# Kernel optimization log

Measured on AMD Instinct MI355X. Metric: run time of the kernel, lower is better.

The kernel has to match this reference:

```python
import jax, jax.numpy as jnp
import numpy as np

E, H, FF, L, S, B = 64, 4, 32, 9, 7, 8192
HD = E // H


def setup_inputs() -> dict:
    key = jax.random.key(0)
    ks = iter(jax.random.split(key, 32))
    def rn(shape, scale=0.05):
        return jax.random.normal(next(ks), shape, dtype=jnp.float32) * scale
    inp = {
        "feature1": jax.random.normal(next(ks), (B, S, E), dtype=jnp.float32),
        "feature2": jax.random.normal(next(ks), (B, S, E), dtype=jnp.float32),
        # branch dim 2: index 0 = rotation, 1 = translation; then layer dim L
        "sa1_win": rn((2, L, 3 * E, E)), "sa1_bin": rn((2, L, 3 * E)),
        "sa1_wout": rn((2, L, E, E)), "sa1_bout": rn((2, L, E)),
        "sa2_win": rn((2, L, 3 * E, E)), "sa2_bin": rn((2, L, 3 * E)),
        "sa2_wout": rn((2, L, E, E)), "sa2_bout": rn((2, L, E)),
        "ca_win": rn((2, L, 3 * E, E)), "ca_bin": rn((2, L, 3 * E)),
        "ca_wout": rn((2, L, E, E)), "ca_bout": rn((2, L, E)),
        "ff_w1": rn((2, L, FF, E)), "ff_b1": rn((2, L, FF)),
        "ff_w2": rn((2, L, E, FF)), "ff_b2": rn((2, L, E)),
        "query_embed": jax.random.normal(next(ks), (2, S, E), dtype=jnp.float32),
        "fc_rot_w": rn((4, E)), "fc_rot_b": rn((4,)),
        "fc_trans_w": rn((3, E)), "fc_trans_b": rn((3,)),
    }
    return inp


def mha(q_in, kv_in, win, b_in, wout, bout):
    # torch nn.MultiheadAttention with batch_first=True
    wq, wk, wv = win[:E], win[E:2 * E], win[2 * E:]
    bq, bk, bv = b_in[:E], b_in[E:2 * E], b_in[2 * E:]
    b, sq, _ = q_in.shape
    sk = kv_in.shape[1]
    q = (q_in @ wq.T + bq).reshape(b, sq, H, HD)
    k = (kv_in @ wk.T + bk).reshape(b, sk, H, HD)
    v = (kv_in @ wv.T + bv).reshape(b, sk, H, HD)
    scores = jnp.einsum("bqhd,bkhd->bhqk", q, k) / jnp.sqrt(jnp.float32(HD))
    attn = jax.nn.softmax(scores, axis=-1)
    ctx = jnp.einsum("bhqk,bkhd->bqhd", attn, v).reshape(b, sq, E)
    return ctx @ wout.T + bout


def _branch(f1, f2, query, bi, sa1_win, sa1_bin, sa1_wout, sa1_bout,
            sa2_win, sa2_bin, sa2_wout, sa2_bout,
            ca_win, ca_bin, ca_wout, ca_bout, ff_w1, ff_b1, ff_w2, ff_b2):
    q = query
    for i in range(L):
        f1 = f1 + mha(f1, f1, sa1_win[bi, i], sa1_bin[bi, i], sa1_wout[bi, i], sa1_bout[bi, i])
        f2 = f2 + mha(f2, f2, sa2_win[bi, i], sa2_bin[bi, i], sa2_wout[bi, i], sa2_bout[bi, i])
        kv = jnp.concatenate([f1, f2], axis=1)  # (B, 2S, E)
        q = q + mha(q, kv, ca_win[bi, i], ca_bin[bi, i], ca_wout[bi, i], ca_bout[bi, i])
        h = jax.nn.relu(q @ ff_w1[bi, i].T + ff_b1[bi, i])
        q = q + h @ ff_w2[bi, i].T + ff_b2[bi, i]
    return q


def reference(feature1, feature2, sa1_win, sa1_bin, sa1_wout, sa1_bout,
              sa2_win, sa2_bin, sa2_wout, sa2_bout,
              ca_win, ca_bin, ca_wout, ca_bout,
              ff_w1, ff_b1, ff_w2, ff_b2, query_embed,
              fc_rot_w, fc_rot_b, fc_trans_w, fc_trans_b):
    b = feature1.shape[0]
    args = (sa1_win, sa1_bin, sa1_wout, sa1_bout, sa2_win, sa2_bin, sa2_wout,
            sa2_bout, ca_win, ca_bin, ca_wout, ca_bout, ff_w1, ff_b1, ff_w2, ff_b2)
    q_rot = jnp.broadcast_to(query_embed[0][None], (b, S, E))
    q_trn = jnp.broadcast_to(query_embed[1][None], (b, S, E))
    # rotation and translation branches are mathematically independent
    rot = _branch(feature1, feature2, q_rot, 0, *args)
    trn = _branch(feature1, feature2, q_trn, 1, *args)
    pose_rot = (rot @ fc_rot_w.T + fc_rot_b).mean(axis=1)    # (B, 4)
    pose_trn = (trn @ fc_trans_w.T + fc_trans_b).mean(axis=1)  # (B, 3)
    return jnp.concatenate([pose_rot, pose_trn], axis=1)  # (B, 7)
```

## Files before the change

kernel.cpp:

```cpp
#include <hip/hip_runtime.h>
#include <hip/hip_bf16.h>

namespace {

using bf16x8 = __attribute__((ext_vector_type(8))) short;
using f32x4  = __attribute__((ext_vector_type(4))) float;

constexpr int NL = 9, S = 7, BB = 8192;
constexpr int G = 8;
constexpr int M = G * S;
constexpr int NT = 512;

constexpr int OFF_F1 = 0;
constexpr int OFF_F2 = 14336;
constexpr int OFF_Q  = 28672;
constexpr int OFF_QB = 43008;
constexpr int OFF_KB = 50176;
constexpr int OFF_VT = 64512;
constexpr int SMEM_TOTAL = 80896;

__device__ __forceinline__ unsigned short f2bf(float f) {
  union { __hip_bfloat16 h; unsigned short s; } u;
  u.h = __float2bfloat16(f);
  return u.s;
}
__device__ __forceinline__ uint32_t pk2(float a, float b) {
  return (uint32_t)f2bf(a) | ((uint32_t)f2bf(b) << 16);
}
__device__ __forceinline__ int swzS(int r, int c) {
  return r * 256 + ((((c >> 3) ^ (r & 7)) << 5) | ((c & 7) << 2));
}
__device__ __forceinline__ int swzB(int r, int c) {
  return r * 128 + ((((c >> 3) ^ (r & 7)) << 4) | ((c & 7) << 1));
}
__device__ __forceinline__ int swzV(int d, int kv) {
  return d * 256 + ((((kv >> 3) ^ (d & 7)) << 4) | ((kv & 7) << 1));
}
__device__ __forceinline__ int div7(int t) { return (t * 9363) >> 16; }

__device__ __forceinline__ bf16x8 ldStateFrag(const char* base, int r, int k0) {
  const float4* p = (const float4*)(base + r * 256 + (((k0 >> 3) ^ (r & 7)) << 5));
  float4 x = p[0], y = p[1];
  union { bf16x8 v; uint32_t u[4]; } o;
  o.u[0] = pk2(x.x, x.y); o.u[1] = pk2(x.z, x.w);
  o.u[2] = pk2(y.x, y.y); o.u[3] = pk2(y.z, y.w);
  return o.v;
}
__device__ __forceinline__ bf16x8 ldBfFrag(const char* base, int r, int k0) {
  return *(const bf16x8*)(base + r * 128 + (((k0 >> 3) ^ (r & 7)) << 4));
}

struct StvNone { __device__ void operator()(int, int, f32x4) const {} };

template <int MTOT, int NTOT, int KF, int WMG, int WNG, int VNT, bool WS,
          class BLD, class STN, class STV>
__device__ __forceinline__ void gemm_sw(const short* __restrict__ wbf,
                                        const float* __restrict__ wf,
                                        const float* __restrict__ bias,
                                        int ldK, int wid, int lane,
                                        BLD bld, STN stn, STV stv)
{
  const int wm = wid / WNG, wn = wid % WNG;
  const int q = lane & 15, gI = lane >> 4;
  constexpr int MPW = (MTOT + WMG - 1) / WMG;
  constexpr int NPW = NTOT / WNG;
  bf16x8 bfr[MPW][KF];
#pragma unroll
  for (int i = 0; i < MPW; ++i) {
    const int mt = wm * MPW + i;
    if (mt < MTOT) {
#pragma unroll
      for (int kf = 0; kf < KF; ++kf)
        bfr[i][kf] = bld(mt * 16 + q, kf * 32 + gI * 8);
    }
  }
#pragma unroll
  for (int j = 0; j < NPW; ++j) {
    const int nt = wn * NPW + j;
    bf16x8 afr[KF];
#pragma unroll
    for (int kf = 0; kf < KF; ++kf) {
      const int k0 = kf * 32 + gI * 8;
      if constexpr (WS) {
        afr[kf] = *(const bf16x8*)(wbf + (size_t)(nt * 16 + q) * ldK + k0);
      } else {
        const float* wp = wf + (size_t)(nt * 16 + q) * ldK + k0;
        float4 x = *(const float4*)wp, y = *(const float4*)(wp + 4);
        union { bf16x8 v; uint32_t u[4]; } o;
        o.u[0] = pk2(x.x, x.y); o.u[1] = pk2(x.z, x.w);
        o.u[2] = pk2(y.x, y.y); o.u[3] = pk2(y.z, y.w);
        afr[kf] = o.v;
      }
    }
    if (nt < VNT) {
      const float4 b4 = *(const float4*)(bias + nt * 16 + gI * 4);
#pragma unroll
      for (int i = 0; i < MPW; ++i) {
        const int mt = wm * MPW + i;
        if (mt < MTOT) {
          f32x4 acc = { b4.x, b4.y, b4.z, b4.w };
#pragma unroll
          for (int kf = 0; kf < KF; ++kf)
            acc = __builtin_amdgcn_mfma_f32_16x16x32_bf16(afr[kf], bfr[i][kf], acc, 0, 0, 0);
          stn(mt, nt, acc);
        }
      }
    } else {
      const float bv = bias[nt * 16 + q];
#pragma unroll
      for (int i = 0; i < MPW; ++i) {
        const int mt = wm * MPW + i;
        if (mt < MTOT) {
          f32x4 acc = { bv, bv, bv, bv };
#pragma unroll
          for (int kf = 0; kf < KF; ++kf)
            acc = __builtin_amdgcn_mfma_f32_16x16x32_bf16(bfr[i][kf], afr[kf], acc, 0, 0, 0);
          stv(mt, nt, acc);
        }
      }
    }
  }
}

template <bool CA_>
__device__ __forceinline__ void attn(char* qb, const char* kb, const char* vt,
                                     int wid, int lane)
{
  const int q = lane & 15, gI = lane >> 4;
  const int g = wid;
  constexpr int KVL = CA_ ? 14 : 7;
#pragma unroll
  for (int h = 0; h < 4; ++h) {
    bf16x8 kfrag = {}, qfrag = {};
    if (gI < 2) {
      int qrow = g * 7 + q; qrow = qrow > 55 ? 55 : qrow;
      qfrag = ldBfFrag(qb, qrow, h * 16 + gI * 8);
      int kvr;
      if constexpr (CA_) {
        kvr = (q < 7) ? (g * 7 + q) : (49 + g * 7 + q);
        kvr = kvr > 111 ? 111 : kvr;
      } else {
        kvr = g * 7 + q; kvr = kvr > 55 ? 55 : kvr;
      }
      kfrag = ldBfFrag(kb, kvr, h * 16 + gI * 8);
    }
    f32x4 s = { 0.f, 0.f, 0.f, 0.f };
    s = __builtin_amdgcn_mfma_f32_16x16x32_bf16(kfrag, qfrag, s, 0, 0, 0);

    float e[4]; float sum = 0.f;
#pragma unroll
    for (int jj = 0; jj < 4; ++jj) {
      const int kvloc = gI * 4 + jj;
      const float tt = fminf(s[jj] * 0.36067376f, 60.f);
      e[jj] = (kvloc < KVL) ? exp2f(tt) : 0.f;
      sum += e[jj];
    }
    sum += __shfl_xor(sum, 16);
    sum += __shfl_xor(sum, 32);
    const float inv = __builtin_amdgcn_rcpf(sum);

    union { bf16x8 v; uint32_t u[4]; } pb;
    pb.u[0] = pk2(e[0] * inv, e[1] * inv);
    pb.u[1] = pk2(e[2] * inv, e[3] * inv);
    pb.u[2] = 0; pb.u[3] = 0;

    const int d = h * 16 + q;
    const int kv0 = (CA_ ? g * 16 : g * 8) + gI * 4;
    const uint2 vv = *(const uint2*)(vt + swzV(d, kv0));
    union { bf16x8 v; uint32_t u[4]; } va;
    va.u[0] = vv.x; va.u[1] = vv.y; va.u[2] = 0; va.u[3] = 0;

    f32x4 o = { 0.f, 0.f, 0.f, 0.f };
    o = __builtin_amdgcn_mfma_f32_16x16x32_bf16(va.v, pb.v, o, 0, 0, 0);

    if (q < 7) {
      const int tok = g * 7 + q, c0 = h * 16 + gI * 4;
      *(uint2*)(qb + swzB(tok, c0)) = make_uint2(pk2(o[0], o[1]), pk2(o[2], o[3]));
    }
  }
}

template <class BLD, bool WS>
__device__ __forceinline__ void out_proj(char* ST, const short* Wo, const float* Fo,
                                         const float* Bo, int wid, int lane, BLD bldc)
{
  const int q = lane & 15, gI = lane >> 4;
  auto stres = [&](int mt, int nt, f32x4 a) {
    const int tok = mt * 16 + q; if (tok >= M) return;
    const int c0 = nt * 16 + gI * 4;
    float4* p = (float4*)(ST + tok * 256 + (((c0 >> 3) ^ (tok & 7)) << 5) + (c0 & 7) * 4);
    float4 v = *p;
    v.x += a[0]; v.y += a[1]; v.z += a[2]; v.w += a[3];
    *p = v;
  };
  gemm_sw<4, 4, 2, 2, 4, 4, WS>(Wo, Fo, Bo, 64, wid, lane, bldc, stres, StvNone{});
}

template <bool WS>
__device__ __forceinline__ void sa_block(char* ST, char* qb, char* kb, char* vt,
    const short* Wi, const float* Fi, const float* Bi,
    const short* Wo, const float* Fo, const float* Bo,
    int wid, int lane)
{
  const int q = lane & 15, gI = lane >> 4;
  auto bld = [&](int r, int k0) { return ldStateFrag(ST, r > 55 ? 55 : r, k0); };
  auto stn = [&](int mt, int nt, f32x4 a) {
    const int tok = mt * 16 + q; if (tok >= M) return;
    if (nt < 4) {
      *(uint2*)(qb + swzB(tok, nt * 16 + gI * 4)) =
          make_uint2(pk2(a[0], a[1]), pk2(a[2], a[3]));
    } else {
      *(uint2*)(kb + swzB(tok, (nt - 4) * 16 + gI * 4)) =
          make_uint2(pk2(a[0], a[1]), pk2(a[2], a[3]));
    }
  };
  auto stv = [&](int mt, int nt, f32x4 a) {
    const int d = (nt - 8) * 16 + q;
#pragma unroll
    for (int jj = 0; jj < 4; ++jj) {
      const int tok = mt * 16 + gI * 4 + jj;
      if (tok < M) {
        const int g = div7(tok);
        *(short*)(vt + swzV(d, g * 8 + (tok - g * 7))) = (short)f2bf(a[jj]);
      }
    }
  };
  gemm_sw<4, 12, 2, 2, 4, 8, WS>(Wi, Fi, Bi, 64, wid, lane, bld, stn, stv);
  __syncthreads();
  attn<false>(qb, kb, vt, wid, lane);
  __syncthreads();
  auto bldc = [&](int r, int k0) { return ldBfFrag(qb, r > 55 ? 55 : r, k0); };
  out_proj<decltype(bldc), WS>(ST, Wo, Fo, Bo, wid, lane, bldc);
  __syncthreads();
}

template <bool WS, int SRC>
__device__ __forceinline__ void ca_kv(const char* SS, char* kb, char* vt,
    const short* Wi, const float* Fi, const float* Bi, int wid, int lane)
{
  const int q = lane & 15, gI = lane >> 4;
  auto bld = [&](int r, int k0) { return ldStateFrag(SS, r > 55 ? 55 : r, k0); };
  auto stk = [&](int mt, int nt, f32x4 a) {
    const int tok = mt * 16 + q; if (tok >= M) return;
    *(uint2*)(kb + swzB(tok + SRC * 56, nt * 16 + gI * 4)) =
        make_uint2(pk2(a[0], a[1]), pk2(a[2], a[3]));
  };
  auto stv = [&](int mt, int nt, f32x4 a) {
    const int d = (nt - 4) * 16 + q;
#pragma unroll
    for (int jj = 0; jj < 4; ++jj) {
      const int tok = mt * 16 + gI * 4 + jj;
      if (tok < M) {
        const int g = div7(tok);
        *(short*)(vt + swzV(d, g * 16 + (tok - g * 7) + SRC * 7)) = (short)f2bf(a[jj]);
      }
    }
  };
  gemm_sw<4, 8, 2, 2, 4, 4, WS>(Wi + 4096, Fi + 4096, Bi + 64, 64, wid, lane,
                                bld, stk, stv);
}

template <bool WS>
__global__ __launch_bounds__(NT, 4) void pose_kernel(
    const float* __restrict__ feature1, const float* __restrict__ feature2,
    const float* __restrict__ sa1_win, const float* __restrict__ sa1_bin,
    const float* __restrict__ sa1_wout, const float* __restrict__ sa1_bout,
    const float* __restrict__ sa2_win, const float* __restrict__ sa2_bin,
    const float* __restrict__ sa2_wout, const float* __restrict__ sa2_bout,
    const float* __restrict__ ca_win, const float* __restrict__ ca_bin,
    const float* __restrict__ ca_wout, const float* __restrict__ ca_bout,
    const float* __restrict__ ff_w1, const float* __restrict__ ff_b1,
    const float* __restrict__ ff_w2, const float* __restrict__ ff_b2,
    const float* __restrict__ query_embed,
    const float* __restrict__ fc_rot_w, const float* __restrict__ fc_rot_b,
    const float* __restrict__ fc_trans_w, const float* __restrict__ fc_trans_b,
    const short* __restrict__ wbf, float* __restrict__ out)
{
  extern __shared__ char smem[];
  char* sF1 = smem + OFF_F1;
  char* sF2 = smem + OFF_F2;
  char* sQ  = smem + OFF_Q;
  char* qb  = smem + OFF_QB;
  char* kb  = smem + OFF_KB;
  char* vt  = smem + OFF_VT;

  const int t = threadIdx.x;
  const int wid = t >> 6, lane = t & 63;
  const int q = lane & 15, gI = lane >> 4;
  const int bi = blockIdx.y;
  const int b0 = blockIdx.x * G;

  {
    const uint4 z = { 0, 0, 0, 0 };
    for (int i = t; i < 1024; i += NT) ((uint4*)vt)[i] = z;
  }
  {
    const float* f1p = feature1 + (size_t)b0 * (S * 64);
    const float* f2p = feature2 + (size_t)b0 * (S * 64);
    const float* qe  = query_embed + (size_t)bi * (S * 64);
    for (int idx = t; idx < M * 64; idx += NT) {
      const int r = idx >> 6, c = idx & 63;
      const int s = r - div7(r) * 7;
      *(float*)(sF1 + swzS(r, c)) = f1p[idx];
      *(float*)(sF2 + swzS(r, c)) = f2p[idx];
      *(float*)(sQ + swzS(r, c))  = qe[s * 64 + c];
    }
  }
  __syncthreads();

  for (int li = 0; li < NL; ++li) {
    const int wo = bi * NL + li;

    sa_block<WS>(sF1, qb, kb, vt,
                 wbf + wo * 12288,          sa1_win + wo * 12288,  sa1_bin + wo * 192,
                 wbf + 663552 + wo * 4096,  sa1_wout + wo * 4096,  sa1_bout + wo * 64,
                 wid, lane);
    sa_block<WS>(sF2, qb, kb, vt,
                 wbf + 221184 + wo * 12288, sa2_win + wo * 12288,  sa2_bin + wo * 192,
                 wbf + 737280 + wo * 4096,  sa2_wout + wo * 4096,  sa2_bout + wo * 64,
                 wid, lane);

    {
      const short* Wi = wbf + 442368 + wo * 12288;
      const float* Fi = ca_win + wo * 12288;
      const float* Bi = ca_bin + wo * 192;
      auto bldq = [&](int r, int k0) { return ldStateFrag(sQ, r > 55 ? 55 : r, k0); };
      auto stq = [&](int mt, int nt, f32x4 a) {
        const int tok = mt * 16 + q; if (tok >= M) return;
        *(uint2*)(qb + swzB(tok, nt * 16 + gI * 4)) =
            make_uint2(pk2(a[0], a[1]), pk2(a[2], a[3]));
      };
      gemm_sw<4, 4, 2, 2, 4, 4, WS>(Wi, Fi, Bi, 64, wid, lane, bldq, stq, StvNone{});
      ca_kv<WS, 0>(sF1, kb, vt, Wi, Fi, Bi, wid, lane);
      ca_kv<WS, 1>(sF2, kb, vt, Wi, Fi, Bi, wid, lane);
      __syncthreads();
      attn<true>(qb, kb, vt, wid, lane);
      __syncthreads();
      auto bldc = [&](int r, int k0) { return ldBfFrag(qb, r > 55 ? 55 : r, k0); };
      out_proj<decltype(bldc), WS>(sQ, wbf + 811008 + wo * 4096, ca_wout + wo * 4096,
                                   ca_bout + wo * 64, wid, lane, bldc);
      __syncthreads();
    }

    {
      auto bldq = [&](int r, int k0) { return ldStateFrag(sQ, r > 55 ? 55 : r, k0); };
      auto sth = [&](int mt, int nt, f32x4 a) {
        const int tok = mt * 16 + q; if (tok >= M) return;
        *(uint2*)(qb + swzB(tok, nt * 16 + gI * 4)) =
            make_uint2(pk2(fmaxf(a[0], 0.f), fmaxf(a[1], 0.f)),
                       pk2(fmaxf(a[2], 0.f), fmaxf(a[3], 0.f)));
      };
      gemm_sw<4, 2, 2, 4, 2, 2, WS>(wbf + 884736 + wo * 2048, ff_w1 + wo * 2048,
                                    ff_b1 + wo * 32, 64, wid, lane, bldq, sth, StvNone{});
      __syncthreads();
      auto bldh = [&](int r, int k0) { return ldBfFrag(qb, r > 55 ? 55 : r, k0); };
      auto stres = [&](int mt, int nt, f32x4 a) {
        const int tok = mt * 16 + q; if (tok >= M) return;
        const int c0 = nt * 16 + gI * 4;
        float4* p = (float4*)(sQ + tok * 256 + (((c0 >> 3) ^ (tok & 7)) << 5) + (c0 & 7) * 4);
        float4 v = *p;
        v.x += a[0]; v.y += a[1]; v.z += a[2]; v.w += a[3];
        *p = v;
      };
      gemm_sw<4, 4, 1, 2, 4, 4, WS>(wbf + 921600 + wo * 2048, ff_w2 + wo * 2048,
                                    ff_b2 + wo * 64, 32, wid, lane, bldh, stres, StvNone{});
      __syncthreads();
    }
  }

  float* cs = (float*)qb;
  {
    const int g = t >> 6, c = t & 63;
    float a = 0.f;
#pragma unroll
    for (int s = 0; s < 7; ++s) a += *(const float*)(sQ + swzS(g * 7 + s, c));
    cs[t] = a;
  }
  __syncthreads();
  const int ncols = bi ? 3 : 4;
  if (t < G * ncols) {
    const int g = t / ncols, cc = t - g * ncols;
    const float* wv = bi ? (fc_trans_w + cc * 64) : (fc_rot_w + cc * 64);
    float acc = 0.f;
#pragma unroll
    for (int k = 0; k < 64; ++k) acc += cs[g * 64 + k] * wv[k];
    const float bb = bi ? fc_trans_b[cc] : fc_rot_b[cc];
    out[(size_t)(b0 + g) * 7 + (bi ? 4 : 0) + cc] = acc * (1.f / 7.f) + bb;
  }
}

__global__ void prep_kernel(const float* __restrict__ a0, const float* __restrict__ a1,
                            const float* __restrict__ a2, const float* __restrict__ a3,
                            const float* __restrict__ a4, const float* __restrict__ a5,
                            const float* __restrict__ a6, const float* __restrict__ a7,
                            short* __restrict__ dst)
{
  for (int i = blockIdx.x * blockDim.x + threadIdx.x; i < 958464;
       i += gridDim.x * blockDim.x) {
    const float* s; int j;
    if      (i < 221184) { s = a0; j = i; }
    else if (i < 442368) { s = a1; j = i - 221184; }
    else if (i < 663552) { s = a2; j = i - 442368; }
    else if (i < 737280) { s = a3; j = i - 663552; }
    else if (i < 811008) { s = a4; j = i - 737280; }
    else if (i < 884736) { s = a5; j = i - 811008; }
    else if (i < 921600) { s = a6; j = i - 884736; }
    else                 { s = a7; j = i - 921600; }
    dst[i] = (short)f2bf(s[j]);
  }
}

}

extern "C" void kernel_launch(void* const* d_in, const int* in_sizes, int n_in,
                              void* d_out, int out_size, void* d_ws, size_t ws_size,
                              hipStream_t stream)
{
  const float* feature1    = (const float*)d_in[0];
  const float* feature2    = (const float*)d_in[1];
  const float* sa1_win     = (const float*)d_in[2];
  const float* sa1_bin     = (const float*)d_in[3];
  const float* sa1_wout    = (const float*)d_in[4];
  const float* sa1_bout    = (const float*)d_in[5];
  const float* sa2_win     = (const float*)d_in[6];
  const float* sa2_bin     = (const float*)d_in[7];
  const float* sa2_wout    = (const float*)d_in[8];
  const float* sa2_bout    = (const float*)d_in[9];
  const float* ca_win      = (const float*)d_in[10];
  const float* ca_bin      = (const float*)d_in[11];
  const float* ca_wout     = (const float*)d_in[12];
  const float* ca_bout     = (const float*)d_in[13];
  const float* ff_w1       = (const float*)d_in[14];
  const float* ff_b1       = (const float*)d_in[15];
  const float* ff_w2       = (const float*)d_in[16];
  const float* ff_b2       = (const float*)d_in[17];
  const float* query_embed = (const float*)d_in[18];
  const float* fc_rot_w    = (const float*)d_in[19];
  const float* fc_rot_b    = (const float*)d_in[20];
  const float* fc_trans_w  = (const float*)d_in[21];
  const float* fc_trans_b  = (const float*)d_in[22];

  const bool ws_ok = (d_ws != nullptr) && (ws_size >= (size_t)958464 * 2);
  dim3 grid(BB / G, 2);

  if (ws_ok) {
    prep_kernel<<<dim3(936), 512, 0, stream>>>(sa1_win, sa2_win, ca_win,
                                               sa1_wout, sa2_wout, ca_wout,
                                               ff_w1, ff_w2, (short*)d_ws);
    hipFuncSetAttribute(reinterpret_cast<const void*>(&pose_kernel<true>),
                        hipFuncAttributeMaxDynamicSharedMemorySize, SMEM_TOTAL);
    pose_kernel<true><<<grid, NT, SMEM_TOTAL, stream>>>(
        feature1, feature2,
        sa1_win, sa1_bin, sa1_wout, sa1_bout,
        sa2_win, sa2_bin, sa2_wout, sa2_bout,
        ca_win, ca_bin, ca_wout, ca_bout,
        ff_w1, ff_b1, ff_w2, ff_b2,
        query_embed, fc_rot_w, fc_rot_b, fc_trans_w, fc_trans_b,
        (const short*)d_ws, (float*)d_out);
  } else {
    hipFuncSetAttribute(reinterpret_cast<const void*>(&pose_kernel<false>),
                        hipFuncAttributeMaxDynamicSharedMemorySize, SMEM_TOTAL);
    pose_kernel<false><<<grid, NT, SMEM_TOTAL, stream>>>(
        feature1, feature2,
        sa1_win, sa1_bin, sa1_wout, sa1_bout,
        sa2_win, sa2_bin, sa2_wout, sa2_bout,
        ca_win, ca_bin, ca_wout, ca_bout,
        ff_w1, ff_b1, ff_w2, ff_b2,
        query_embed, fc_rot_w, fc_rot_b, fc_trans_w, fc_trans_b,
        (const short*)d_ws, (float*)d_out);
  }
}
```

Baseline: 1.350 ms.

## Give each wavefront its own batch sample and drop block-wide barriers

Restructures the kernel so each of the 8 waves in a block processes one batch element independently, with its own LDS region. Block-level __syncthreads are replaced by compiler memory fences, and the V layout and attention masking are simplified for a single sample. Each wave now runs all N-tiles of every GEMM on one 16-row M tile with only 7 valid rows, which wastes more MFMA work per sample and multiplies weight fragment loads per sample. In exchange it removes cross-wave synchronization. The final pose head is also reduced with wave shuffles.

Measured after the change: 2.342 ms. +73.5%, slower.

```diff
diff --git a/kernel.cpp b/kernel.cpp
--- a/kernel.cpp
+++ b/kernel.cpp
@@ -1,23 +1,25 @@
 #include <hip/hip_runtime.h>
 #include <hip/hip_bf16.h>
 
+#define WAVE_FENCE() asm volatile("" ::: "memory")
+
 namespace {
 
 using bf16x8 = __attribute__((ext_vector_type(8))) short;
 using f32x4  = __attribute__((ext_vector_type(4))) float;
 
-constexpr int NL = 9, S = 7, BB = 8192;
-constexpr int G = 8;
-constexpr int M = G * S;
-constexpr int NT = 512;
-
-constexpr int OFF_F1 = 0;
-constexpr int OFF_F2 = 14336;
-constexpr int OFF_Q  = 28672;
-constexpr int OFF_QB = 43008;
-constexpr int OFF_KB = 50176;
-constexpr int OFF_VT = 64512;
-constexpr int SMEM_TOTAL = 80896;
+constexpr int NL = 9, BB = 8192;
+constexpr int WPB = 8;
+constexpr int NT = 64 * WPB;
+
+constexpr int WV_F1 = 0;
+constexpr int WV_F2 = 1792;
+constexpr int WV_SQ = 3584;
+constexpr int WV_QB = 5376;
+constexpr int WV_KB = 6272;
+constexpr int WV_VT = 8192;
+constexpr int WVSZ  = 10240;
+constexpr int SMEM_TOTAL = WVSZ * WPB;
 
 __device__ __forceinline__ unsigned short f2bf(float f) {
   union { __hip_bfloat16 h; unsigned short s; } u;
@@ -33,10 +35,6 @@
 __device__ __forceinline__ int swzB(int r, int c) {
   return r * 128 + ((((c >> 3) ^ (r & 7)) << 4) | ((c & 7) << 1));
 }
-__device__ __forceinline__ int swzV(int d, int kv) {
-  return d * 256 + ((((kv >> 3) ^ (d & 7)) << 4) | ((kv & 7) << 1));
-}
-__device__ __forceinline__ int div7(int t) { return (t * 9363) >> 16; }
 
 __device__ __forceinline__ bf16x8 ldStateFrag(const char* base, int r, int k0) {
   const float4* p = (const float4*)(base + r * 256 + (((k0 >> 3) ^ (r & 7)) << 5));
@@ -47,126 +45,112 @@
   return o.v;
 }
 __device__ __forceinline__ bf16x8 ldBfFrag(const char* base, int r, int k0) {
-  return *(const bf16x8*)(base + r * 128 + (((k0 >> 3) ^ (r & 7)) << 4));
-}
-
-struct StvNone { __device__ void operator()(int, int, f32x4) const {} };
-
-template <int MTOT, int NTOT, int KF, int WMG, int WNG, int VNT, bool WS,
-          class BLD, class STN, class STV>
-__device__ __forceinline__ void gemm_sw(const short* __restrict__ wbf,
-                                        const float* __restrict__ wf,
-                                        const float* __restrict__ bias,
-                                        int ldK, int wid, int lane,
-                                        BLD bld, STN stn, STV stv)
-{
-  const int wm = wid / WNG, wn = wid % WNG;
-  const int q = lane & 15, gI = lane >> 4;
-  constexpr int MPW = (MTOT + WMG - 1) / WMG;
-  constexpr int NPW = NTOT / WNG;
-  bf16x8 bfr[MPW][KF];
+  const uint2* p = (const uint2*)(base + r * 128 + (((k0 >> 3) ^ (r & 7)) << 4));
+  const uint2 a = p[0], b = p[1];
+  union { bf16x8 v; uint32_t u[4]; } o;
+  o.u[0] = a.x; o.u[1] = a.y; o.u[2] = b.x; o.u[3] = b.y;
+  return o.v;
+}
+
+template <int NTOT, int KF, int VNT, bool WS, class BLD, class STN, class STV>
+__device__ __forceinline__ void gemmw(const short* __restrict__ wbf,
+                                      const float* __restrict__ wf,
+                                      const float* __restrict__ biasN,
+                                      const float* __restrict__ biasV,
+                                      int q, int gI, BLD bld, STN stn, STV stv)
+{
+  constexpr int LDK = (KF == 2) ? 64 : 32;
+  const bf16x8 b0 = bld(q, gI * 8);
+  bf16x8 b1 = b0;
+  if constexpr (KF == 2) b1 = bld(q, 32 + gI * 8);
 #pragma unroll
-  for (int i = 0; i < MPW; ++i) {
-    const int mt = wm * MPW + i;
-    if (mt < MTOT) {
-#pragma unroll
-      for (int kf = 0; kf < KF; ++kf)
-        bfr[i][kf] = bld(mt * 16 + q, kf * 32 + gI * 8);
-    }
-  }
-#pragma unroll
-  for (int j = 0; j < NPW; ++j) {
-    const int nt = wn * NPW + j;
-    bf16x8 afr[KF];
-#pragma unroll
-    for (int kf = 0; kf < KF; ++kf) {
-      const int k0 = kf * 32 + gI * 8;
-      if constexpr (WS) {
-        afr[kf] = *(const bf16x8*)(wbf + (size_t)(nt * 16 + q) * ldK + k0);
-      } else {
-        const float* wp = wf + (size_t)(nt * 16 + q) * ldK + k0;
+  for (int nt = 0; nt < NTOT; ++nt) {
+    const int row = nt * 16 + q;
+    bf16x8 a0, a1;
+    if constexpr (WS) {
+      a0 = *(const bf16x8*)(wbf + row * LDK + gI * 8);
+      if constexpr (KF == 2)
+        a1 = *(const bf16x8*)(wbf + row * LDK + 32 + gI * 8);
+    } else {
+      {
+        const float* wp = wf + row * LDK + gI * 8;
         float4 x = *(const float4*)wp, y = *(const float4*)(wp + 4);
         union { bf16x8 v; uint32_t u[4]; } o;
         o.u[0] = pk2(x.x, x.y); o.u[1] = pk2(x.z, x.w);
         o.u[2] = pk2(y.x, y.y); o.u[3] = pk2(y.z, y.w);
-        afr[kf] = o.v;
+        a0 = o.v;
       }
+      a1 = a0;
+      if constexpr (KF == 2) {
+        const float* wp = wf + row * LDK + 32 + gI * 8;
+        float4 x = *(const float4*)wp, y = *(const float4*)(wp + 4);
+        union { bf16x8 v; uint32_t u[4]; } o;
+        o.u[0] = pk2(x.x, x.y); o.u[1] = pk2(x.z, x.w);
+        o.u[2] = pk2(y.x, y.y); o.u[3] = pk2(y.z, y.w);
+        a1 = o.v;
+      }
     }
     if (nt < VNT) {
-      const float4 b4 = *(const float4*)(bias + nt * 16 + gI * 4);
-#pragma unroll
-      for (int i = 0; i < MPW; ++i) {
-        const int mt = wm * MPW + i;
-        if (mt < MTOT) {
-          f32x4 acc = { b4.x, b4.y, b4.z, b4.w };
-#pragma unroll
-          for (int kf = 0; kf < KF; ++kf)
-            acc = __builtin_amdgcn_mfma_f32_16x16x32_bf16(afr[kf], bfr[i][kf], acc, 0, 0, 0);
-          stn(mt, nt, acc);
-        }
-      }
+      const float4 b4 = *(const float4*)(biasN + nt * 16 + gI * 4);
+      f32x4 acc = { b4.x, b4.y, b4.z, b4.w };
+      acc = __builtin_amdgcn_mfma_f32_16x16x32_bf16(a0, b0, acc, 0, 0, 0);
+      if constexpr (KF == 2)
+        acc = __builtin_amdgcn_mfma_f32_16x16x32_bf16(a1, b1, acc, 0, 0, 0);
+      stn(nt, acc);
     } else {
-      const float bv = bias[nt * 16 + q];
-#pragma unroll
-      for (int i = 0; i < MPW; ++i) {
-        const int mt = wm * MPW + i;
-        if (mt < MTOT) {
-          f32x4 acc = { bv, bv, bv, bv };
-#pragma unroll
-          for (int kf = 0; kf < KF; ++kf)
-            acc = __builtin_amdgcn_mfma_f32_16x16x32_bf16(bfr[i][kf], afr[kf], acc, 0, 0, 0);
-          stv(mt, nt, acc);
-        }
-      }
+      const float bv = biasV[(nt - VNT) * 16 + q];
+      f32x4 acc = { bv, bv, bv, bv };
+      acc = __builtin_amdgcn_mfma_f32_16x16x32_bf16(b0, a0, acc, 0, 0, 0);
+      if constexpr (KF == 2)
+        acc = __builtin_amdgcn_mfma_f32_16x16x32_bf16(b1, a1, acc, 0, 0, 0);
+      stv(nt - VNT, acc);
     }
   }
 }
 
 template <bool CA_>
-__device__ __forceinline__ void attn(char* qb, const char* kb, const char* vt,
-                                     int wid, int lane)
-{
-  const int q = lane & 15, gI = lane >> 4;
-  const int g = wid;
-  constexpr int KVL = CA_ ? 14 : 7;
+__device__ __forceinline__ void attnw(char* qb, const char* kb, const char* vt,
+                                      int q, int gI)
+{
+  constexpr int KCL = CA_ ? 14 : 6;
 #pragma unroll
   for (int h = 0; h < 4; ++h) {
     bf16x8 kfrag = {}, qfrag = {};
     if (gI < 2) {
-      int qrow = g * 7 + q; qrow = qrow > 55 ? 55 : qrow;
-      qfrag = ldBfFrag(qb, qrow, h * 16 + gI * 8);
-      int kvr;
-      if constexpr (CA_) {
-        kvr = (q < 7) ? (g * 7 + q) : (49 + g * 7 + q);
-        kvr = kvr > 111 ? 111 : kvr;
-      } else {
-        kvr = g * 7 + q; kvr = kvr > 55 ? 55 : kvr;
-      }
-      kfrag = ldBfFrag(kb, kvr, h * 16 + gI * 8);
+      qfrag = ldBfFrag(qb, q > 6 ? 6 : q, h * 16 + gI * 8);
+      kfrag = ldBfFrag(kb, q > KCL ? KCL : q, h * 16 + gI * 8);
     }
     f32x4 s = { 0.f, 0.f, 0.f, 0.f };
     s = __builtin_amdgcn_mfma_f32_16x16x32_bf16(kfrag, qfrag, s, 0, 0, 0);
 
-    float e[4]; float sum = 0.f;
-#pragma unroll
-    for (int jj = 0; jj < 4; ++jj) {
-      const int kvloc = gI * 4 + jj;
-      const float tt = fminf(s[jj] * 0.36067376f, 60.f);
-      e[jj] = (kvloc < KVL) ? exp2f(tt) : 0.f;
-      sum += e[jj];
+    float e0, e1, e2, e3, sum;
+    {
+      const int k0 = gI * 4;
+      const float t0 = fminf(s[0] * 0.36067376f, 60.f);
+      const float t1 = fminf(s[1] * 0.36067376f, 60.f);
+      const float t2 = fminf(s[2] * 0.36067376f, 60.f);
+      const float t3 = fminf(s[3] * 0.36067376f, 60.f);
+      const bool v0 = CA_ ? (((k0 + 0) & 7) < 7) : (k0 + 0 < 7);
+      const bool v1 = CA_ ? (((k0 + 1) & 7) < 7) : (k0 + 1 < 7);
+      const bool v2 = CA_ ? (((k0 + 2) & 7) < 7) : (k0 + 2 < 7);
+      const bool v3 = CA_ ? (((k0 + 3) & 7) < 7) : (k0 + 3 < 7);
+      e0 = v0 ? exp2f(t0) : 0.f;
+      e1 = v1 ? exp2f(t1) : 0.f;
+      e2 = v2 ? exp2f(t2) : 0.f;
+      e3 = v3 ? exp2f(t3) : 0.f;
+      sum = e0 + e1 + e2 + e3;
     }
     sum += __shfl_xor(sum, 16);
     sum += __shfl_xor(sum, 32);
     const float inv = __builtin_amdgcn_rcpf(sum);
 
     union { bf16x8 v; uint32_t u[4]; } pb;
-    pb.u[0] = pk2(e[0] * inv, e[1] * inv);
-    pb.u[1] = pk2(e[2] * inv, e[3] * inv);
+    pb.u[0] = pk2(e0 * inv, e1 * inv);
+    pb.u[1] = pk2(e2 * inv, e3 * inv);
     pb.u[2] = 0; pb.u[3] = 0;
 
     const int d = h * 16 + q;
-    const int kv0 = (CA_ ? g * 16 : g * 8) + gI * 4;
-    const uint2 vv = *(const uint2*)(vt + swzV(d, kv0));
+    const uint2 vv = *(const uint2*)(vt + d * 32 + gI * 8);
     union { bf16x8 v; uint32_t u[4]; } va;
     va.u[0] = vv.x; va.u[1] = vv.y; va.u[2] = 0; va.u[3] = 0;
 
@@ -174,90 +158,63 @@
     o = __builtin_amdgcn_mfma_f32_16x16x32_bf16(va.v, pb.v, o, 0, 0, 0);
 
     if (q < 7) {
-      const int tok = g * 7 + q, c0 = h * 16 + gI * 4;
-      *(uint2*)(qb + swzB(tok, c0)) = make_uint2(pk2(o[0], o[1]), pk2(o[2], o[3]));
-    }
-  }
-}
-
-template <class BLD, bool WS>
-__device__ __forceinline__ void out_proj(char* ST, const short* Wo, const float* Fo,
-                                         const float* Bo, int wid, int lane, BLD bldc)
-{
-  const int q = lane & 15, gI = lane >> 4;
-  auto stres = [&](int mt, int nt, f32x4 a) {
-    const int tok = mt * 16 + q; if (tok >= M) return;
+      *(uint2*)(qb + swzB(q, h * 16 + gI * 4)) =
+          make_uint2(pk2(o[0], o[1]), pk2(o[2], o[3]));
+    }
+  }
+}
+
+template <bool WS>
+__device__ __forceinline__ void sa_blockw(char* ST, char* qb, char* kb, char* vt,
+    const short* Wi, const float* Fi, const float* Bi,
+    const short* Wo, const float* Fo, const float* Bo, int q, int gI)
+{
+  auto bld = [&](int r, int k0) { return ldStateFrag(ST, r > 6 ? 6 : r, k0); };
+  auto stn = [&](int nt, f32x4 a) {
+    if (q >= 7) return;
+    const uint2 v = make_uint2(pk2(a[0], a[1]), pk2(a[2], a[3]));
+    if (nt < 4) *(uint2*)(qb + swzB(q, nt * 16 + gI * 4)) = v;
+    else        *(uint2*)(kb + swzB(q, (nt - 4) * 16 + gI * 4)) = v;
+  };
+  auto stv = [&](int ntv, f32x4 a) {
+    const int d = ntv * 16 + q;
+    *(uint2*)(vt + d * 32 + gI * 8) = make_uint2(pk2(a[0], a[1]), pk2(a[2], a[3]));
+  };
+  gemmw<12, 2, 8, WS>(Wi, Fi, Bi, Bi + 128, q, gI, bld, stn, stv);
+  WAVE_FENCE();
+  attnw<false>(qb, kb, vt, q, gI);
+  WAVE_FENCE();
+  auto bldc = [&](int r, int k0) { return ldBfFrag(qb, r > 6 ? 6 : r, k0); };
+  auto stres = [&](int nt, f32x4 a) {
+    if (q >= 7) return;
     const int c0 = nt * 16 + gI * 4;
-    float4* p = (float4*)(ST + tok * 256 + (((c0 >> 3) ^ (tok & 7)) << 5) + (c0 & 7) * 4);
+    float4* p = (float4*)(ST + q * 256 + (((c0 >> 3) ^ (q & 7)) << 5) + ((c0 & 7) << 2));
     float4 v = *p;
     v.x += a[0]; v.y += a[1]; v.z += a[2]; v.w += a[3];
     *p = v;
   };
-  gemm_sw<4, 4, 2, 2, 4, 4, WS>(Wo, Fo, Bo, 64, wid, lane, bldc, stres, StvNone{});
-}
-
-template <bool WS>
-__device__ __forceinline__ void sa_block(char* ST, char* qb, char* kb, char* vt,
-    const short* Wi, const float* Fi, const float* Bi,
-    const short* Wo, const float* Fo, const float* Bo,
-    int wid, int lane)
-{
-  const int q = lane & 15, gI = lane >> 4;
-  auto bld = [&](int r, int k0) { return ldStateFrag(ST, r > 55 ? 55 : r, k0); };
-  auto stn = [&](int mt, int nt, f32x4 a) {
-    const int tok = mt * 16 + q; if (tok >= M) return;
-    if (nt < 4) {
-      *(uint2*)(qb + swzB(tok, nt * 16 + gI * 4)) =
-          make_uint2(pk2(a[0], a[1]), pk2(a[2], a[3]));
-    } else {
-      *(uint2*)(kb + swzB(tok, (nt - 4) * 16 + gI * 4)) =
-          make_uint2(pk2(a[0], a[1]), pk2(a[2], a[3]));
-    }
-  };
-  auto stv = [&](int mt, int nt, f32x4 a) {
-    const int d = (nt - 8) * 16 + q;
-#pragma unroll
-    for (int jj = 0; jj < 4; ++jj) {
-      const int tok = mt * 16 + gI * 4 + jj;
-      if (tok < M) {
-        const int g = div7(tok);
-        *(short*)(vt + swzV(d, g * 8 + (tok - g * 7))) = (short)f2bf(a[jj]);
-      }
-    }
-  };
-  gemm_sw<4, 12, 2, 2, 4, 8, WS>(Wi, Fi, Bi, 64, wid, lane, bld, stn, stv);
-  __syncthreads();
-  attn<false>(qb, kb, vt, wid, lane);
-  __syncthreads();
-  auto bldc = [&](int r, int k0) { return ldBfFrag(qb, r > 55 ? 55 : r, k0); };
-  out_proj<decltype(bldc), WS>(ST, Wo, Fo, Bo, wid, lane, bldc);
-  __syncthreads();
+  auto dum = [](int, f32x4) {};
+  gemmw<4, 2, 4, WS>(Wo, Fo, Bo, Bo, q, gI, bldc, stres, dum);
+  WAVE_FENCE();
 }
 
 template <bool WS, int SRC>
-__device__ __forceinline__ void ca_kv(const char* SS, char* kb, char* vt,
-    const short* Wi, const float* Fi, const float* Bi, int wid, int lane)
-{
-  const int q = lane & 15, gI = lane >> 4;
-  auto bld = [&](int r, int k0) { return ldStateFrag(SS, r > 55 ? 55 : r, k0); };
-  auto stk = [&](int mt, int nt, f32x4 a) {
-    const int tok = mt * 16 + q; if (tok >= M) return;
-    *(uint2*)(kb + swzB(tok + SRC * 56, nt * 16 + gI * 4)) =
+__device__ __forceinline__ void ca_kvw(const char* SS, char* kb, char* vt,
+    const short* Wi, const float* Fi, const float* Bi, int q, int gI)
+{
+  auto bld = [&](int r, int k0) { return ldStateFrag(SS, r > 6 ? 6 : r, k0); };
+  auto stk = [&](int nt, f32x4 a) {
+    if (q >= 7) return;
+    *(uint2*)(kb + swzB(q + SRC * 8, nt * 16 + gI * 4)) =
         make_uint2(pk2(a[0], a[1]), pk2(a[2], a[3]));
   };
-  auto stv = [&](int mt, int nt, f32x4 a) {
-    const int d = (nt - 4) * 16 + q;
-#pragma unroll
-    for (int jj = 0; jj < 4; ++jj) {
-      const int tok = mt * 16 + gI * 4 + jj;
-      if (tok < M) {
-        const int g = div7(tok);
-        *(short*)(vt + swzV(d, g * 16 + (tok - g * 7) + SRC * 7)) = (short)f2bf(a[jj]);
-      }
-    }
+  auto stv = [&](int ntv, f32x4 a) {
+    if (gI >= 2) return;
+    const int d = ntv * 16 + q;
+    *(uint2*)(vt + d * 32 + gI * 8 + SRC * 16) =
+        make_uint2(pk2(a[0], a[1]), pk2(a[2], a[3]));
   };
-  gemm_sw<4, 8, 2, 2, 4, 4, WS>(Wi + 4096, Fi + 4096, Bi + 64, 64, wid, lane,
-                                bld, stk, stv);
+  gemmw<8, 2, 4, WS>(Wi + 4096, Fi + 4096, Bi + 64, Bi + 128, q, gI, bld, stk, stv);
 }
 
 template <bool WS>
@@ -277,115 +234,121 @@
     const short* __restrict__ wbf, float* __restrict__ out)
 {
   extern __shared__ char smem[];
-  char* sF1 = smem + OFF_F1;
-  char* sF2 = smem + OFF_F2;
-  char* sQ  = smem + OFF_Q;
-  char* qb  = smem + OFF_QB;
-  char* kb  = smem + OFF_KB;
-  char* vt  = smem + OFF_VT;
-
   const int t = threadIdx.x;
   const int wid = t >> 6, lane = t & 63;
   const int q = lane & 15, gI = lane >> 4;
   const int bi = blockIdx.y;
-  const int b0 = blockIdx.x * G;
+  const int sidx = blockIdx.x * WPB + wid;
+
+  char* wb = smem + wid * WVSZ;
+  char* F1_ = wb + WV_F1;
+  char* F2_ = wb + WV_F2;
+  char* SQ_ = wb + WV_SQ;
+  char* qb  = wb + WV_QB;
+  char* kb  = wb + WV_KB;
+  char* vt  = wb + WV_VT;
 
   {
     const uint4 z = { 0, 0, 0, 0 };
-    for (int i = t; i < 1024; i += NT) ((uint4*)vt)[i] = z;
+    for (int i = lane; i < 304; i += 64) ((uint4*)(wb + WV_QB))[i] = z;
   }
   {
-    const float* f1p = feature1 + (size_t)b0 * (S * 64);
-    const float* f2p = feature2 + (size_t)b0 * (S * 64);
-    const float* qe  = query_embed + (size_t)bi * (S * 64);
-    for (int idx = t; idx < M * 64; idx += NT) {
-      const int r = idx >> 6, c = idx & 63;
-      const int s = r - div7(r) * 7;
-      *(float*)(sF1 + swzS(r, c)) = f1p[idx];
-      *(float*)(sF2 + swzS(r, c)) = f2p[idx];
-      *(float*)(sQ + swzS(r, c))  = qe[s * 64 + c];
-    }
-  }
-  __syncthreads();
+    const float* f1p = feature1 + (size_t)sidx * 448;
+    const float* f2p = feature2 + (size_t)sidx * 448;
+    const float* qe  = query_embed + (size_t)bi * 448;
+    for (int i = lane; i < 448; i += 64) {
+      const int r = i >> 6, c = i & 63;
+      *(float*)(F1_ + swzS(r, c)) = f1p[i];
+      *(float*)(F2_ + swzS(r, c)) = f2p[i];
+      *(float*)(SQ_ + swzS(r, c)) = qe[i];
+    }
+  }
+  WAVE_FENCE();
+
+  auto dum = [](int, f32x4) {};
 
   for (int li = 0; li < NL; ++li) {
     const int wo = bi * NL + li;
 
-    sa_block<WS>(sF1, qb, kb, vt,
-                 wbf + wo * 12288,          sa1_win + wo * 12288,  sa1_bin + wo * 192,
-                 wbf + 663552 + wo * 4096,  sa1_wout + wo * 4096,  sa1_bout + wo * 64,
-                 wid, lane);
-    sa_block<WS>(sF2, qb, kb, vt,
-                 wbf + 221184 + wo * 12288, sa2_win + wo * 12288,  sa2_bin + wo * 192,
-                 wbf + 737280 + wo * 4096,  sa2_wout + wo * 4096,  sa2_bout + wo * 64,
-                 wid, lane);
+    sa_blockw<WS>(F1_, qb, kb, vt,
+                  wbf + wo * 12288,          sa1_win + wo * 12288,  sa1_bin + wo * 192,
+                  wbf + 663552 + wo * 4096,  sa1_wout + wo * 4096,  sa1_bout + wo * 64,
+                  q, gI);
+    sa_blockw<WS>(F2_, qb, kb, vt,
+                  wbf + 221184 + wo * 12288, sa2_win + wo * 12288,  sa2_bin + wo * 192,
+                  wbf + 737280 + wo * 4096,  sa2_wout + wo * 4096,  sa2_bout + wo * 64,
+                  q, gI);
 
     {
       const short* Wi = wbf + 442368 + wo * 12288;
       const float* Fi = ca_win + wo * 12288;
       const float* Bi = ca_bin + wo * 192;
-      auto bldq = [&](int r, int k0) { return ldStateFrag(sQ, r > 55 ? 55 : r, k0); };
-      auto stq = [&](int mt, int nt, f32x4 a) {
-        const int tok = mt * 16 + q; if (tok >= M) return;
-        *(uint2*)(qb + swzB(tok, nt * 16 + gI * 4)) =
+      auto bldq = [&](int r, int k0) { return ldStateFrag(SQ_, r > 6 ? 6 : r, k0); };
+      auto stq = [&](int nt, f32x4 a) {
+        if (q >= 7) return;
+        *(uint2*)(qb + swzB(q, nt * 16 + gI * 4)) =
             make_uint2(pk2(a[0], a[1]), pk2(a[2], a[3]));
       };
-      gemm_sw<4, 4, 2, 2, 4, 4, WS>(Wi, Fi, Bi, 64, wid, lane, bldq, stq, StvNone{});
-      ca_kv<WS, 0>(sF1, kb, vt, Wi, Fi, Bi, wid, lane);
-      ca_kv<WS, 1>(sF2, kb, vt, Wi, Fi, Bi, wid, lane);
-      __syncthreads();
-      attn<true>(qb, kb, vt, wid, lane);
-      __syncthreads();
-      auto bldc = [&](int r, int k0) { return ldBfFrag(qb, r > 55 ? 55 : r, k0); };
-      out_proj<decltype(bldc), WS>(sQ, wbf + 811008 + wo * 4096, ca_wout + wo * 4096,
-                                   ca_bout + wo * 64, wid, lane, bldc);
-      __syncthreads();
-    }
-
-    {
-      auto bldq = [&](int r, int k0) { return ldStateFrag(sQ, r > 55 ? 55 : r, k0); };
-      auto sth = [&](int mt, int nt, f32x4 a) {
-        const int tok = mt * 16 + q; if (tok >= M) return;
-        *(uint2*)(qb + swzB(tok, nt * 16 + gI * 4)) =
-            make_uint2(pk2(fmaxf(a[0], 0.f), fmaxf(a[1], 0.f)),
-                       pk2(fmaxf(a[2], 0.f), fmaxf(a[3], 0.f)));
-      };
-      gemm_sw<4, 2, 2, 4, 2, 2, WS>(wbf + 884736 + wo * 2048, ff_w1 + wo * 2048,
-                                    ff_b1 + wo * 32, 64, wid, lane, bldq, sth, StvNone{});
-      __syncthreads();
-      auto bldh = [&](int r, int k0) { return ldBfFrag(qb, r > 55 ? 55 : r, k0); };
-      auto stres = [&](int mt, int nt, f32x4 a) {
-        const int tok = mt * 16 + q; if (tok >= M) return;
+      gemmw<4, 2, 4, WS>(Wi, Fi, Bi, Bi, q, gI, bldq, stq, dum);
+      ca_kvw<WS, 0>(F1_, kb, vt, Wi, Fi, Bi, q, gI);
+      ca_kvw<WS, 1>(F2_, kb, vt, Wi, Fi, Bi, q, gI);
+      WAVE_FENCE();
+      attnw<true>(qb, kb, vt, q, gI);
+      WAVE_FENCE();
+      auto bldc = [&](int r, int k0) { return ldBfFrag(qb, r > 6 ? 6 : r, k0); };
+      auto stres = [&](int nt, f32x4 a) {
+        if (q >= 7) return;
         const int c0 = nt * 16 + gI * 4;
-        float4* p = (float4*)(sQ + tok * 256 + (((c0 >> 3) ^ (tok & 7)) << 5) + (c0 & 7) * 4);
+        float4* p = (float4*)(SQ_ + q * 256 + (((c0 >> 3) ^ (q & 7)) << 5) + ((c0 & 7) << 2));
         float4 v = *p;
         v.x += a[0]; v.y += a[1]; v.z += a[2]; v.w += a[3];
         *p = v;
       };
-      gemm_sw<4, 4, 1, 2, 4, 4, WS>(wbf + 921600 + wo * 2048, ff_w2 + wo * 2048,
-                                    ff_b2 + wo * 64, 32, wid, lane, bldh, stres, StvNone{});
-      __syncthreads();
-    }
-  }
-
-  float* cs = (float*)qb;
+      gemmw<4, 2, 4, WS>(wbf + 811008 + wo * 4096, ca_wout + wo * 4096,
+                         ca_bout + wo * 64, ca_bout + wo * 64, q, gI, bldc, stres, dum);
+      WAVE_FENCE();
+    }
+
+    {
+      auto bldq = [&](int r, int k0) { return ldStateFrag(SQ_, r > 6 ? 6 : r, k0); };
+      auto sth = [&](int nt, f32x4 a) {
+        if (q >= 7) return;
+        *(uint2*)(qb + swzB(q, nt * 16 + gI * 4)) =
+            make_uint2(pk2(fmaxf(a[0], 0.f), fmaxf(a[1], 0.f)),
+                       pk2(fmaxf(a[2], 0.f), fmaxf(a[3], 0.f)));
+      };
+      gemmw<2, 2, 2, WS>(wbf + 884736 + wo * 2048, ff_w1 + wo * 2048,
+                         ff_b1 + wo * 32, ff_b1 + wo * 32, q, gI, bldq, sth, dum);
+      WAVE_FENCE();
+      auto bldh = [&](int r, int k0) { return ldBfFrag(qb, r > 6 ? 6 : r, k0); };
+      auto stres = [&](int nt, f32x4 a) {
+        if (q >= 7) return;
+        const int c0 = nt * 16 + gI * 4;
+        float4* p = (float4*)(SQ_ + q * 256 + (((c0 >> 3) ^ (q & 7)) << 5) + ((c0 & 7) << 2));
+        float4 v = *p;
+        v.x += a[0]; v.y += a[1]; v.z += a[2]; v.w += a[3];
+        *p = v;
+      };
+      gemmw<4, 1, 4, WS>(wbf + 921600 + wo * 2048, ff_w2 + wo * 2048,
+                         ff_b2 + wo * 64, ff_b2 + wo * 64, q, gI, bldh, stres, dum);
+      WAVE_FENCE();
+    }
+  }
+
   {
-    const int g = t >> 6, c = t & 63;
-    float a = 0.f;
+    float cs = 0.f;
 #pragma unroll
-    for (int s = 0; s < 7; ++s) a += *(const float*)(sQ + swzS(g * 7 + s, c));
-    cs[t] = a;
-  }
-  __syncthreads();
-  const int ncols = bi ? 3 : 4;
-  if (t < G * ncols) {
-    const int g = t / ncols, cc = t - g * ncols;
-    const float* wv = bi ? (fc_trans_w + cc * 64) : (fc_rot_w + cc * 64);
-    float acc = 0.f;
-#pragma unroll
-    for (int k = 0; k < 64; ++k) acc += cs[g * 64 + k] * wv[k];
-    const float bb = bi ? fc_trans_b[cc] : fc_rot_b[cc];
-    out[(size_t)(b0 + g) * 7 + (bi ? 4 : 0) + cc] = acc * (1.f / 7.f) + bb;
+    for (int s = 0; s < 7; ++s) cs += *(const float*)(SQ_ + swzS(s, lane));
+    const int ncols = bi ? 3 : 4;
+    const float* W  = bi ? fc_trans_w : fc_rot_w;
+    const float* Bv = bi ? fc_trans_b : fc_rot_b;
+    for (int cc = 0; cc < ncols; ++cc) {
+      float p = cs * W[cc * 64 + lane];
+      p += __shfl_xor(p, 1);  p += __shfl_xor(p, 2);  p += __shfl_xor(p, 4);
+      p += __shfl_xor(p, 8);  p += __shfl_xor(p, 16); p += __shfl_xor(p, 32);
+      if (lane == 0)
+        out[(size_t)sidx * 7 + (bi ? 4 : 0) + cc] = p * (1.f / 7.f) + Bv[cc];
+    }
   }
 }
 
@@ -441,7 +404,7 @@
   const float* fc_trans_b  = (const float*)d_in[22];
 
   const bool ws_ok = (d_ws != nullptr) && (ws_size >= (size_t)958464 * 2);
-  dim3 grid(BB / G, 2);
+  dim3 grid(BB / WPB, 2);
 
   if (ws_ok) {
     prep_kernel<<<dim3(936), 512, 0, stream>>>(sa1_win, sa2_win, ca_win,
```
